# Kernel tuning notes

Measured on AMD Instinct MI355X. Metric: run time of the kernel, lower is better.

## Reference

```python
import jax, jax.numpy as jnp
import numpy as np

IN_FEATURES = 4096
OUT_FEATURES = 768
N_BITS = 8
BATCH = 4096


def setup_inputs() -> dict:
    key = jax.random.key(0)
    k1, k2, k3 = jax.random.split(key, 3)
    latent = jax.random.uniform(k1, (BATCH, IN_FEATURES), dtype=jnp.float32)
    true_sum = jax.random.uniform(k2, (BATCH, OUT_FEATURES * N_BITS), dtype=jnp.float32)
    # kaiming-normal-ish init: std = sqrt(2 / fan_in)
    weight = jax.random.normal(k3, (IN_FEATURES, OUT_FEATURES * N_BITS), dtype=jnp.float32) * np.sqrt(2.0 / IN_FEATURES)
    return {"latent": latent, "true_sum": true_sum, "weight": weight, "n_bits": N_BITS}


def reference(latent, true_sum, weight, n_bits):
    in_features = weight.shape[0]
    batch = latent.shape[0]
    # powers of two, MSB negated (two's-complement style decode)
    powers = (2.0 ** jnp.arange(n_bits, dtype=jnp.float32))
    powers = powers.at[-1].multiply(-1.0)

    prob_weights = jax.nn.sigmoid(weight)                      # [in, out*n_bits]
    # decode soft bits -> integer-valued weights: [in, out]
    int_weights = (prob_weights.reshape(in_features, -1, n_bits) * powers).sum(-1)
    # decode target bits -> integer-valued sums: [batch, out]
    int_sum = (true_sum.reshape(batch, -1, n_bits) * powers).sum(-1)

    # (latent.unsqueeze(-1) * int_weights).sum(-2) is exactly a GEMM
    pred = latent @ int_weights                                # [batch, out]

    scale_factor = 2.0 ** (n_bits - 1)
    recon_loss = jnp.mean((pred - int_sum) ** 2) / scale_factor
    polarize_loss = jnp.mean(prob_weights * (1.0 - prob_weights))
    return (recon_loss, polarize_loss)
```

## Files before the change

kernel.cpp:

```cpp
#include <hip/hip_runtime.h>
#include <stdint.h>

#define IN_F   4096
#define OUT_F  768
#define NB     8
#define BATCH  4096
#define WCOLS  (OUT_F*NB)

typedef short  bf16x8  __attribute__((ext_vector_type(8)));
typedef float  f32x4   __attribute__((ext_vector_type(4)));
typedef unsigned short ushort8 __attribute__((ext_vector_type(8)));

__device__ __forceinline__ unsigned short f2bf(float f){
    union { float f; uint32_t u; } v; v.f = f;
    uint32_t u = v.u;
    u += 0x7FFFu + ((u >> 16) & 1u);
    return (unsigned short)(u >> 16);
}

__device__ __forceinline__ void gload16(const void* g, void* l){
    __builtin_amdgcn_global_load_lds(
        (const __attribute__((address_space(1))) unsigned int*)g,
        (__attribute__((address_space(3))) unsigned int*)l, 16, 0, 0);
}

__global__ void prep_latent(const float* __restrict__ lat,
                            unsigned short* __restrict__ abf,
                            float* __restrict__ acc){
    if (blockIdx.x == 0 && threadIdx.x < 4) acc[threadIdx.x] = 0.f;
    int idx = (blockIdx.x * 256 + threadIdx.x) * 8;
    const float4* p = (const float4*)(lat + idx);
    float4 a = p[0], b = p[1];
    ushort8 o;
    o[0]=f2bf(a.x); o[1]=f2bf(a.y); o[2]=f2bf(a.z); o[3]=f2bf(a.w);
    o[4]=f2bf(b.x); o[5]=f2bf(b.y); o[6]=f2bf(b.z); o[7]=f2bf(b.w);
    *(ushort8*)(abf + idx) = o;
}

__global__ void decode_weight(const float* __restrict__ w,
                              unsigned short* __restrict__ bt,
                              float* __restrict__ acc){
    __shared__ unsigned short tile[64][70];
    __shared__ float part[4];
    const int tid = threadIdx.x;
    const int k0 = blockIdx.x * 64;
    const int n0 = blockIdx.y * 64;
    const int j     = tid & 63;
    const int ibase = (tid >> 6) * 16;
    float pol = 0.f;
    #pragma unroll 4
    for (int r = 0; r < 16; ++r){
        int i = ibase + r;
        const float4* src = (const float4*)(w + (size_t)(k0+i)*WCOLS + (size_t)(n0+j)*8);
        float4 a = src[0], b = src[1];
        float x[8] = {a.x,a.y,a.z,a.w,b.x,b.y,b.z,b.w};
        float p[8];
        #pragma unroll
        for (int q = 0; q < 8; ++q){
            p[q] = 1.f / (1.f + __expf(-x[q]));
            pol += p[q] * (1.f - p[q]);
        }
        float iw = p[0] + 2.f*p[1] + 4.f*p[2] + 8.f*p[3]
                 + 16.f*p[4] + 32.f*p[5] + 64.f*p[6] - 128.f*p[7];
        tile[j][i] = f2bf(iw);
    }
    #pragma unroll
    for (int off = 32; off; off >>= 1) pol += __shfl_down(pol, off);
    if ((tid & 63) == 0) part[tid >> 6] = pol;
    __syncthreads();
    const int nrow = tid >> 4;
    const int kb   = (tid & 15) * 4;
    #pragma unroll
    for (int q = 0; q < 4; ++q){
        int n = nrow + q*16;
        uint2 v;
        v.x = *(const unsigned int*)&tile[n][kb];
        v.y = *(const unsigned int*)&tile[n][kb+2];
        *(uint2*)(bt + (size_t)(n0+n)*IN_F + k0 + kb) = v;
    }
    if (tid == 0) atomicAdd(&acc[1], part[0]+part[1]+part[2]+part[3]);
}

#define BM 128
#define BN 128
#define BK 64

__launch_bounds__(512)
__global__ void gemm_loss(const unsigned short* __restrict__ abf,
                          const unsigned short* __restrict__ bt,
                          const float* __restrict__ ts,
                          float* __restrict__ acc){
    __shared__ unsigned short As[BM*BK];
    __shared__ unsigned short Bs[BN*BK];
    __shared__ float part[8];
    const int tid = threadIdx.x;
    const int w   = tid >> 6;
    const int l   = tid & 63;
    const int s   = l & 15, g = l >> 4;
    const int sw  = s & 7;
    const int wr  = w >> 2, wc = w & 3;
    const int m0  = blockIdx.x * BM;
    const int n0  = blockIdx.y * BN;

    f32x4 accv[4][2];
    #pragma unroll
    for (int m = 0; m < 4; ++m)
        #pragma unroll
        for (int n = 0; n < 2; ++n)
            accv[m][n] = (f32x4){0.f,0.f,0.f,0.f};

    const int srow = tid >> 3;
    const int sc   = tid & 7;
    const int swz  = ((sc ^ (srow & 7)) << 3);
    const unsigned short* aSrc0 = abf + (size_t)(m0 + srow)     * IN_F + swz;
    const unsigned short* aSrc1 = abf + (size_t)(m0 + 64 + srow)* IN_F + swz;
    const unsigned short* bSrc0 = bt  + (size_t)(n0 + srow)     * IN_F + swz;
    const unsigned short* bSrc1 = bt  + (size_t)(n0 + 64 + srow)* IN_F + swz;
    char* AsB = (char*)As;
    char* BsB = (char*)Bs;
    const int wbase = w * 1024;

    const int arow = wr*64 + s;
    const int bcol = wc*32 + s;

    for (int kt = 0; kt < IN_F/BK; ++kt){
        const int ko = kt * BK;
        gload16(aSrc0 + ko, AsB + wbase);
        gload16(aSrc1 + ko, AsB + 8192 + wbase);
        gload16(bSrc0 + ko, BsB + wbase);
        gload16(bSrc1 + ko, BsB + 8192 + wbase);
        __syncthreads();
        #pragma unroll
        for (int kk = 0; kk < 2; ++kk){
            bf16x8 af[4], bfr[2];
            const int chunk = ((kk*4 + g) ^ sw) << 4;
            #pragma unroll
            for (int m = 0; m < 4; ++m)
                af[m] = *(const bf16x8*)(AsB + (arow + m*16)*128 + chunk);
            #pragma unroll
            for (int n = 0; n < 2; ++n)
                bfr[n] = *(const bf16x8*)(BsB + (bcol + n*16)*128 + chunk);
            #pragma unroll
            for (int m = 0; m < 4; ++m)
                #pragma unroll
                for (int n = 0; n < 2; ++n)
                    accv[m][n] = __builtin_amdgcn_mfma_f32_16x16x32_bf16(
                        af[m], bfr[n], accv[m][n], 0, 0, 0);
        }
        __syncthreads();
    }

    float local = 0.f;
    #pragma unroll
    for (int m = 0; m < 4; ++m){
        int rbase = m0 + wr*64 + m*16 + g*4;
        #pragma unroll
        for (int n = 0; n < 2; ++n){
            int col = n0 + wc*32 + n*16 + s;
            const float* tsp = ts + (size_t)rbase*WCOLS + (size_t)col*8;
            #pragma unroll
            for (int jj = 0; jj < 4; ++jj){
                const float4* q = (const float4*)(tsp + (size_t)jj*WCOLS);
                float4 x = q[0], y = q[1];
                float isum = x.x + 2.f*x.y + 4.f*x.z + 8.f*x.w
                           + 16.f*y.x + 32.f*y.y + 64.f*y.z - 128.f*y.w;
                float d = accv[m][n][jj] - isum;
                local += d*d;
            }
        }
    }
    #pragma unroll
    for (int off = 32; off; off >>= 1) local += __shfl_down(local, off);
    if (l == 0) part[w] = local;
    __syncthreads();
    if (tid == 0){
        float ssum = 0.f;
        #pragma unroll
        for (int i = 0; i < 8; ++i) ssum += part[i];
        atomicAdd(&acc[0], ssum);
    }
}

__global__ void finalize(const float* __restrict__ acc, float* __restrict__ out){
    out[0] = acc[0] * (1.0f / ((float)BATCH * (float)OUT_F * 128.0f));
    out[1] = acc[1] * (1.0f / ((float)IN_F * (float)WCOLS));
}

extern "C" void kernel_launch(void* const* d_in, const int* in_sizes, int n_in,
                              void* d_out, int out_size, void* d_ws, size_t ws_size,
                              hipStream_t stream){
    const float* latent   = (const float*)d_in[0];
    const float* true_sum = (const float*)d_in[1];
    const float* weight   = (const float*)d_in[2];
    float* acc = (float*)d_ws;
    unsigned short* abf = (unsigned short*)((char*)d_ws + 1024);
    unsigned short* bt  = (unsigned short*)((char*)d_ws + 1024 + (size_t)BATCH*IN_F*2);
    float* out = (float*)d_out;

    prep_latent<<<(BATCH*IN_F)/(256*8), 256, 0, stream>>>(latent, abf, acc);
    decode_weight<<<dim3(IN_F/64, OUT_F/64), 256, 0, stream>>>(weight, bt, acc);
    gemm_loss<<<dim3(BATCH/BM, OUT_F/BN), 512, 0, stream>>>(abf, bt, true_sum, acc);
    finalize<<<1, 1, 0, stream>>>(acc, out);
}
```

Measured before the change: 120.2 us.

## Double-buffer GEMM LDS tiles and retile to 128x96 with 4 waves

The GEMM now double-buffers the A and B shared-memory tiles so the async global-to-LDS loads for the next K step are issued before computing the current one. This replaces the load/sync/compute/sync pattern. The block tile changes from 128x128 to 128x96 with 256 threads, so each wave computes a 64x48 sub-tile with 12 MFMAs per k-step. The grid becomes 32x8 = 256 blocks, matching the CU count. The cost is more LDS per block and higher per-wave register pressure, which may reduce occupancy.

New measurement: 125.1 us. 4.1% more time.

```diff
diff --git a/kernel.cpp b/kernel.cpp
--- a/kernel.cpp
+++ b/kernel.cpp
@@ -82,72 +82,90 @@
 }
 
 #define BM 128
-#define BN 128
+#define BN 96
 #define BK 64
-
-__launch_bounds__(512)
+#define NT (IN_F/BK)
+#define ABYTES (BM*BK*2)
+#define BBYTES (BN*BK*2)
+
+__launch_bounds__(256)
 __global__ void gemm_loss(const unsigned short* __restrict__ abf,
                           const unsigned short* __restrict__ bt,
                           const float* __restrict__ ts,
                           float* __restrict__ acc){
-    __shared__ unsigned short As[BM*BK];
-    __shared__ unsigned short Bs[BN*BK];
-    __shared__ float part[8];
+    __shared__ unsigned short As[2][BM*BK];
+    __shared__ unsigned short Bs[2][BN*BK];
+    __shared__ float part[4];
     const int tid = threadIdx.x;
     const int w   = tid >> 6;
     const int l   = tid & 63;
     const int s   = l & 15, g = l >> 4;
-    const int sw  = s & 7;
-    const int wr  = w >> 2, wc = w & 3;
+    const int wr  = w >> 1, wc = w & 1;
     const int m0  = blockIdx.x * BM;
     const int n0  = blockIdx.y * BN;
 
-    f32x4 accv[4][2];
+    f32x4 accv[4][3];
     #pragma unroll
     for (int m = 0; m < 4; ++m)
         #pragma unroll
-        for (int n = 0; n < 2; ++n)
+        for (int n = 0; n < 3; ++n)
             accv[m][n] = (f32x4){0.f,0.f,0.f,0.f};
 
-    const int srow = tid >> 3;
-    const int sc   = tid & 7;
-    const int swz  = ((sc ^ (srow & 7)) << 3);
-    const unsigned short* aSrc0 = abf + (size_t)(m0 + srow)     * IN_F + swz;
-    const unsigned short* aSrc1 = abf + (size_t)(m0 + 64 + srow)* IN_F + swz;
-    const unsigned short* bSrc0 = bt  + (size_t)(n0 + srow)     * IN_F + swz;
-    const unsigned short* bSrc1 = bt  + (size_t)(n0 + 64 + srow)* IN_F + swz;
+    const int c8  = tid & 7;
+    const int r0  = tid >> 3;
+    const int scw = ((c8 ^ (r0 & 7)) << 3);
+    const unsigned short* aS = abf + (size_t)(m0 + r0) * IN_F + scw;
+    const unsigned short* bS = bt  + (size_t)(n0 + r0) * IN_F + scw;
     char* AsB = (char*)As;
     char* BsB = (char*)Bs;
-    const int wbase = w * 1024;
-
-    const int arow = wr*64 + s;
-    const int bcol = wc*32 + s;
-
-    for (int kt = 0; kt < IN_F/BK; ++kt){
-        const int ko = kt * BK;
-        gload16(aSrc0 + ko, AsB + wbase);
-        gload16(aSrc1 + ko, AsB + 8192 + wbase);
-        gload16(bSrc0 + ko, BsB + wbase);
-        gload16(bSrc1 + ko, BsB + 8192 + wbase);
+
+    #define STAGE(kt, b) do {                                              \
+        const int _ko = (kt) * BK;                                         \
+        char* _ad = AsB + (b)*ABYTES + tid*16;                             \
+        char* _bd = BsB + (b)*BBYTES + tid*16;                             \
+        _Pragma("unroll")                                                  \
+        for (int _i = 0; _i < 4; ++_i)                                     \
+            gload16(aS + (size_t)_i*32*IN_F + _ko, _ad + _i*4096);         \
+        _Pragma("unroll")                                                  \
+        for (int _i = 0; _i < 3; ++_i)                                     \
+            gload16(bS + (size_t)_i*32*IN_F + _ko, _bd + _i*4096);         \
+    } while (0)
+
+    #define COMPUTE(b) do {                                                \
+        char* _Ab = AsB + (b)*ABYTES;                                      \
+        char* _Bb = BsB + (b)*BBYTES;                                      \
+        _Pragma("unroll")                                                  \
+        for (int _kk = 0; _kk < 2; ++_kk){                                 \
+            bf16x8 _af[4], _bf[3];                                         \
+            _Pragma("unroll")                                              \
+            for (int _m = 0; _m < 4; ++_m){                                \
+                int _r  = wr*64 + _m*16 + s;                               \
+                int _ch = _r*8 + ((_kk*4 + g) ^ (_r & 7));                 \
+                _af[_m] = *(const bf16x8*)(_Ab + _ch*16);                  \
+            }                                                              \
+            _Pragma("unroll")                                              \
+            for (int _n = 0; _n < 3; ++_n){                                \
+                int _r  = wc*48 + _n*16 + s;                               \
+                int _ch = _r*8 + ((_kk*4 + g) ^ (_r & 7));                 \
+                _bf[_n] = *(const bf16x8*)(_Bb + _ch*16);                  \
+            }                                                              \
+            _Pragma("unroll")                                              \
+            for (int _m = 0; _m < 4; ++_m)                                 \
+                _Pragma("unroll")                                          \
+                for (int _n = 0; _n < 3; ++_n)                             \
+                    accv[_m][_n] = __builtin_amdgcn_mfma_f32_16x16x32_bf16(\
+                        _af[_m], _bf[_n], accv[_m][_n], 0, 0, 0);          \
+        }                                                                  \
+    } while (0)
+
+    STAGE(0, 0);
+    __syncthreads();
+    int cur = 0;
+    for (int kt = 0; kt < NT; ++kt){
+        if (kt + 1 < NT) STAGE(kt + 1, cur ^ 1);
+        COMPUTE(cur);
         __syncthreads();
-        #pragma unroll
-        for (int kk = 0; kk < 2; ++kk){
-            bf16x8 af[4], bfr[2];
-            const int chunk = ((kk*4 + g) ^ sw) << 4;
-            #pragma unroll
-            for (int m = 0; m < 4; ++m)
-                af[m] = *(const bf16x8*)(AsB + (arow + m*16)*128 + chunk);
-            #pragma unroll
-            for (int n = 0; n < 2; ++n)
-                bfr[n] = *(const bf16x8*)(BsB + (bcol + n*16)*128 + chunk);
-            #pragma unroll
-            for (int m = 0; m < 4; ++m)
-                #pragma unroll
-                for (int n = 0; n < 2; ++n)
-                    accv[m][n] = __builtin_amdgcn_mfma_f32_16x16x32_bf16(
-                        af[m], bfr[n], accv[m][n], 0, 0, 0);
-        }
-        __syncthreads();
+        cur ^= 1;
     }
 
     float local = 0.f;
@@ -155,8 +173,8 @@
     for (int m = 0; m < 4; ++m){
         int rbase = m0 + wr*64 + m*16 + g*4;
         #pragma unroll
-        for (int n = 0; n < 2; ++n){
-            int col = n0 + wc*32 + n*16 + s;
+        for (int n = 0; n < 3; ++n){
+            int col = n0 + wc*48 + n*16 + s;
             const float* tsp = ts + (size_t)rbase*WCOLS + (size_t)col*8;
             #pragma unroll
             for (int jj = 0; jj < 4; ++jj){
@@ -174,10 +192,7 @@
     if (l == 0) part[w] = local;
     __syncthreads();
     if (tid == 0){
-        float ssum = 0.f;
-        #pragma unroll
-        for (int i = 0; i < 8; ++i) ssum += part[i];
-        atomicAdd(&acc[0], ssum);
+        atomicAdd(&acc[0], part[0]+part[1]+part[2]+part[3]);
     }
 }
 
@@ -199,6 +214,6 @@
 
     prep_latent<<<(BATCH*IN_F)/(256*8), 256, 0, stream>>>(latent, abf, acc);
     decode_weight<<<dim3(IN_F/64, OUT_F/64), 256, 0, stream>>>(weight, bt, acc);
-    gemm_loss<<<dim3(BATCH/BM, OUT_F/BN), 512, 0, stream>>>(abf, bt, true_sum, acc);
+    gemm_loss<<<dim3(BATCH/BM, OUT_F/BN), 256, 0, stream>>>(abf, bt, true_sum, acc);
     finalize<<<1, 1, 0, stream>>>(acc, out);
 }
```
